# Kernel optimization log

Measured on AMD Instinct MI355X. Metric: run time of the kernel, lower is better.

The kernel has to match this reference:

```python
import jax, jax.numpy as jnp
import numpy as np

B, T, I, H, NSHIFT = 64, 1024, 128, 512, 32


def setup_inputs() -> dict:
    key = jax.random.key(0)
    ks = jax.random.split(key, 8)
    s_in = 1.0 / np.sqrt(I)
    s_h = 1.0 / np.sqrt(H)
    return {
        "x": jax.random.normal(ks[0], (B, T, I), dtype=jnp.float32),
        "W1": jax.random.uniform(ks[1], (I, H), minval=-s_in, maxval=s_in, dtype=jnp.float32),
        "b1": jax.random.uniform(ks[2], (H,), minval=-s_in, maxval=s_in, dtype=jnp.float32),
        "W_ih": jax.random.uniform(ks[3], (H, 4 * H), minval=-s_h, maxval=s_h, dtype=jnp.float32),
        "W_hh": jax.random.uniform(ks[4], (H, 4 * H), minval=-s_h, maxval=s_h, dtype=jnp.float32),
        "b_lstm": jax.random.uniform(ks[5], (4 * H,), minval=-s_h, maxval=s_h, dtype=jnp.float32),
        "Wo": jax.random.uniform(ks[6], (H, NSHIFT), minval=-s_h, maxval=s_h, dtype=jnp.float32),
        "bo": jax.random.uniform(ks[7], (NSHIFT,), minval=-s_h, maxval=s_h, dtype=jnp.float32),
    }


def _lstm_scan(xs, W_ih, W_hh, b, hidden):
    # xs: [T, B, H] (time-major for scan). Sine activation replaces tanh.
    Bsz = xs.shape[1]
    h0 = jnp.zeros((Bsz, hidden), dtype=xs.dtype)
    c0 = jnp.zeros((Bsz, hidden), dtype=xs.dtype)

    def step(carry, xt):
        h, c = carry
        gates = xt @ W_ih + h @ W_hh + b  # [B, 4H]
        i, f, g, o = jnp.split(gates, 4, axis=-1)
        i = jax.nn.sigmoid(i)
        f = jax.nn.sigmoid(f)
        g = jnp.sin(g)  # sine activation in place of tanh
        o = jax.nn.sigmoid(o)
        c_new = f * c + i * g
        h_new = o * jnp.sin(c_new)
        return (h_new, c_new), h_new

    (hT, cT), hs = jax.lax.scan(step, (h0, c0), xs)
    return hs, (hT, cT)


def reference(x, W1, b1, W_ih, W_hh, b_lstm, Wo, bo):
    # fc1: [B, T, I] -> [B, T, H]
    fc1_out = x @ W1 + b1
    xs = jnp.swapaxes(fc1_out, 0, 1)  # [T, B, H]
    hs, _ = _lstm_scan(xs, W_ih, W_hh, b_lstm, W_hh.shape[0])
    lstm_out = jnp.swapaxes(hs, 0, 1)  # [B, T, H]
    return lstm_out @ Wo + bo  # [B, T, n_shift]
```

## Files before the change

### kernel.cpp

```cpp
#include <hip/hip_runtime.h>


constexpr int Bb = 64;
constexpr int Tt = 1024;
constexpr int Ii = 128;
constexpr int Hh = 512;
constexpr int G4 = 2048;
constexpr int NS = 32;
constexpr int NG = 16;
constexpr int GW = 16;
constexpr int BPG = 4;

typedef _Float16 h2 __attribute__((ext_vector_type(2)));
typedef _Float16 h8 __attribute__((ext_vector_type(8)));
typedef float    f4 __attribute__((ext_vector_type(4)));
typedef unsigned int u32;
typedef u32 u32x2 __attribute__((ext_vector_type(2)));
typedef u32 u32x4 __attribute__((ext_vector_type(4)));

__device__ __forceinline__ float dot8(h8 w, h8 x, float acc) {
  h2 w0 = {w[0], w[1]}, w1 = {w[2], w[3]}, w2 = {w[4], w[5]}, w3 = {w[6], w[7]};
  h2 x0 = {x[0], x[1]}, x1 = {x[2], x[3]}, x2 = {x[4], x[5]}, x3 = {x[6], x[7]};
  acc = __builtin_amdgcn_fdot2(x0, w0, acc, false);
  acc = __builtin_amdgcn_fdot2(x1, w1, acc, false);
  acc = __builtin_amdgcn_fdot2(x2, w2, acc, false);
  acc = __builtin_amdgcn_fdot2(x3, w3, acc, false);
  return acc;
}

__device__ __forceinline__ float sigf(float x) { return 1.f / (1.f + __expf(-x)); }


__global__ void k_wc(const float* __restrict__ W1, const float* __restrict__ Wih,
                     const float* __restrict__ b1, const float* __restrict__ bl,
                     _Float16* __restrict__ Wc4, float* __restrict__ bias2) {
  const int j = blockIdx.x;
  const int i = threadIdx.x;
  __shared__ float col[Hh];
  __shared__ float part[128];
  for (int k = i; k < Hh; k += 128) col[k] = Wih[k * G4 + j];
  __syncthreads();
  float s = 0.f;
  for (int k = i; k < Hh; k += 128) s += b1[k] * col[k];
  part[i] = s;
  __syncthreads();
  if (i == 0) {
    float t = bl[j];
    for (int k = 0; k < 128; k++) t += part[k];
    bias2[j] = t;
  }
  float acc = 0.f;
  const float* w1r = W1 + i * Hh;
#pragma unroll 4
  for (int k = 0; k < Hh; k++) acc += w1r[k] * col[k];
  const int gate = j >> 9, r = j & 511, ss = r >> 5, u = r & 31;
  const int c128 = gate * 32 + u, cb = c128 >> 4, c = c128 & 15;
  const int lane = ((i >> 3) & 3) * 16 + c, ks4 = i >> 5, e = i & 7;
  Wc4[((ss * 8 + cb) * 4 + ks4) * 512 + lane * 8 + e] = (_Float16)acc;
}

__global__ void k_whh(const float* __restrict__ W, _Float16* __restrict__ W4) {
  const int id = blockIdx.x * 256 + threadIdx.x;
  const int lane = id & 63, ks = (id >> 6) & 15, cb = (id >> 10) & 7, ss = id >> 13;
  const int c = lane & 15, c128 = cb * 16 + c;
  const int gate = c128 >> 5, u = c128 & 31;
  const int colg = gate * 512 + ss * 32 + u;
  h8 o;
#pragma unroll
  for (int e = 0; e < 8; ++e)
    o[e] = (_Float16)W[(ks * 32 + (lane >> 4) * 8 + e) * G4 + colg];
  *(h8*)(W4 + ((ss * 8 + cb) * 16 + ks) * 512 + lane * 8) = o;
}

__global__ __launch_bounds__(512, 1) void k_scan(
    const float* __restrict__ x, const _Float16* __restrict__ Wc4,
    const float* __restrict__ bias2, const _Float16* __restrict__ Whh4,
    const float* __restrict__ Wo, const float* __restrict__ bo,
    float* __restrict__ out, char* __restrict__ hpub) {
  const int gid = blockIdx.x >> 4, ss = blockIdx.x & 15;
  const int tid = threadIdx.x;
  const int lane = tid & 63, wv = tid >> 6;
  const int l15 = lane & 15, l4 = lane >> 4;

  __shared__ __align__(16) char hls[2][16384];
  __shared__ __align__(16) char xws[4096];
  __shared__ __align__(16) char wots[32768];
  __shared__ float pre_s[2][2][4][4][33];
  __shared__ float gat_s[4][4][33];
  __shared__ float op_s[32][17];

  h8 bW[16], bC[4];
#pragma unroll
  for (int ks = 0; ks < 16; ++ks)
    bW[ks] = *(const h8*)(Whh4 + ((ss * 8 + wv) * 16 + ks) * 512 + lane * 8);
#pragma unroll
  for (int ks = 0; ks < 4; ++ks)
    bC[ks] = *(const h8*)(Wc4 + ((ss * 8 + wv) * 4 + ks) * 512 + lane * 8);

  const int b8 = tid >> 5, ml = tid & 31;
  const float bI = bias2[ss * 32 + ml],        bF = bias2[512 + ss * 32 + ml],
              bG = bias2[1024 + ss * 32 + ml], bO = bias2[1536 + ss * 32 + ml];
  const int nn = tid & 31, pp = tid >> 5;
  const float bor = (tid < NS) ? bo[tid] : 0.f;

#pragma unroll
  for (int q = 0; q < 2; ++q) {
    u32x4 z = {0, 0, 0, 0};
    *(u32x4*)(hls[0] + (q * 512 + tid) * 16) = z;
    *(u32x4*)(hls[1] + (q * 512 + tid) * 16) = z;
  }
  if (tid < 256) { u32x4 z = {0, 0, 0, 0}; *(u32x4*)(xws + tid * 16) = z; }
  for (int it = tid; it < Hh * NS; it += 512) {
    int k = it >> 5, n = it & 31;
    *(_Float16*)(wots + n * 1024 + ((2 * k) ^ ((n & 7) << 4))) = (_Float16)Wo[k * NS + n];
  }
  float c_ = 0.f;

  auto stage_x = [&](int t0) {
    if (tid < 128) {
      const int row = tid >> 4, cc = tid & 15;
      const float* src = x + ((size_t)(gid * BPG + (row & 3)) * Tt + t0 + (row >> 2)) * Ii + cc * 8;
      f4 s0 = *(const f4*)src, s1 = *(const f4*)(src + 4);
      h8 v = {(_Float16)s0[0], (_Float16)s0[1], (_Float16)s0[2], (_Float16)s0[3],
              (_Float16)s1[0], (_Float16)s1[1], (_Float16)s1[2], (_Float16)s1[3]};
      *(h8*)(xws + row * 256 + ((cc * 16) ^ ((row & 7) << 4))) = v;
    }
  };
  auto do_pregate = [&](int buf) {
    f4 pa = {0.f, 0.f, 0.f, 0.f};
#pragma unroll
    for (int ks = 0; ks < 4; ++ks) {
      const int row = l15;
      h8 a = *(const h8*)(xws + row * 256 + ((ks * 64 + l4 * 16) ^ ((row & 7) << 4)));
      pa = __builtin_amdgcn_mfma_f32_16x16x32_f16(a, bC[ks], pa, 0, 0, 0);
    }
    if (l4 < 2) {
      const int c128 = wv * 16 + l15, gam = c128 >> 5, u = c128 & 31;
#pragma unroll
      for (int e = 0; e < 4; ++e) {
        const int row = l4 * 4 + e;
        pre_s[buf][row >> 2][row & 3][gam][u] = pa[e];
      }
    }
  };
  auto op_part = [&](const char* hb) {
    if (ss < BPG) {
      float acc = 0.f;
#pragma unroll
      for (int q = 0; q < 4; ++q) {
        h8 w_ = *(const h8*)(wots + nn * 1024 + ((pp * 64 + q * 16) ^ ((nn & 7) << 4)));
        h8 hv = *(const h8*)(hb + ss * 1024 + ((pp * 64 + q * 16) ^ (ss << 4)));
        acc = dot8(w_, hv, acc);
      }
      op_s[nn][pp] = acc;
    }
  };

  stage_x(0);
  __syncthreads();
  do_pregate(0);

  int cur = 0;
#pragma unroll 1
  for (int t = 0; t < Tt; ++t) {
    char* const hpg = hpub + gid * 16384 + (t & 1) * 8192;
    const char* const hc = hls[cur];
    char* const hn_ = hls[cur ^ 1];
    {
      f4 g0 = {0.f, 0.f, 0.f, 0.f}, g1 = {0.f, 0.f, 0.f, 0.f};
#pragma unroll
      for (int ks = 0; ks < 16; ++ks) {
        const int row = l15;
        h8 a = *(const h8*)(hc + row * 1024 + ((ks * 64 + l4 * 16) ^ (row << 4)));
        if (ks & 1) g1 = __builtin_amdgcn_mfma_f32_16x16x32_f16(a, bW[ks], g1, 0, 0, 0);
        else        g0 = __builtin_amdgcn_mfma_f32_16x16x32_f16(a, bW[ks], g0, 0, 0, 0);
      }
      if (l4 == 0) {
        const int c128 = wv * 16 + l15, gam = c128 >> 5, u = c128 & 31;
#pragma unroll
        for (int e = 0; e < 4; ++e) gat_s[e][gam][u] = g0[e] + g1[e];
      }
    }
    __syncthreads();
    if (tid < 128) {
      const int ph = (t >> 1) & 1, tt = t & 1;
      float aI = gat_s[b8][0][ml] + pre_s[ph][tt][b8][0][ml] + bI;
      float aF = gat_s[b8][1][ml] + pre_s[ph][tt][b8][1][ml] + bF;
      float aG = gat_s[b8][2][ml] + pre_s[ph][tt][b8][2][ml] + bG;
      float aO = gat_s[b8][3][ml] + pre_s[ph][tt][b8][3][ml] + bO;
      float iv = sigf(aI), fv = sigf(aF), gv = __sinf(aG), ov = sigf(aO);
      c_ = fv * c_ + iv * gv;
      float hnv = ov * __sinf(c_);
      _Float16 hf = (_Float16)hnv;
      u32 pkt = (u32)__builtin_bit_cast(unsigned short, hf) | ((u32)(t + 1) << 16);
      u32* dst = (u32*)(hpg + ((size_t)(b8 * 512 + ss * 32 + ml)) * 4);
      asm volatile("global_store_dword %0, %1, off sc0 sc1" :: "v"(dst), "v"(pkt) : "memory");
    }
    if (!(t & 1)) { if (t <= 1020) stage_x(t + 2); }
    else if (t <= 1021) do_pregate(((t + 1) >> 1) & 1);
    if (t > 0) op_part(hc);
    {
      const u32* sp = (const u32*)(hpg + (size_t)tid * 16);
      const u32 want = (u32)(t + 1);
      u32x4 v;
      while (true) {
        asm volatile("global_load_dwordx4 %0, %1, off sc0 sc1\ns_waitcnt vmcnt(0)"
                     : "=v"(v) : "v"(sp) : "memory");
        if ((v[0] >> 16) == want && (v[1] >> 16) == want &&
            (v[2] >> 16) == want && (v[3] >> 16) == want) break;
      }
      __builtin_amdgcn_sched_barrier(0);
      u32x2 d = {(v[0] & 0xFFFFu) | (v[1] << 16), (v[2] & 0xFFFFu) | (v[3] << 16)};
      const int b = tid >> 7, k = tid & 127;
      *(u32x2*)(hn_ + b * 1024 + ((k * 8) ^ (b << 4))) = d;
    }
    __syncthreads();
    if (t > 0 && ss < BPG && tid < NS) {
      float s_ = bor;
#pragma unroll
      for (int p = 0; p < 16; ++p) s_ += op_s[tid][p];
      out[((size_t)(gid * BPG + ss) * Tt + (t - 1)) * NS + tid] = s_;
    }
    cur ^= 1;
  }
  op_part(hls[cur]);
  __syncthreads();
  if (ss < BPG && tid < NS) {
    float s_ = bor;
#pragma unroll
    for (int p = 0; p < 16; ++p) s_ += op_s[tid][p];
    out[((size_t)(gid * BPG + ss) * Tt + 1023) * NS + tid] = s_;
  }
}

extern "C" void kernel_launch(void* const* d_in, const int* in_sizes, int n_in,
                              void* d_out, int out_size, void* d_ws, size_t ws_size,
                              hipStream_t stream) {
  const float* x   = (const float*)d_in[0];
  const float* W1  = (const float*)d_in[1];
  const float* b1  = (const float*)d_in[2];
  const float* Wih = (const float*)d_in[3];
  const float* Whh = (const float*)d_in[4];
  const float* bl  = (const float*)d_in[5];
  const float* Wo  = (const float*)d_in[6];
  const float* bo  = (const float*)d_in[7];
  float* out = (float*)d_out;

  char* ws = (char*)d_ws;
  _Float16* Wc4   = (_Float16*)(ws);
  float*    bias2 = (float*)(ws + 524288);
  _Float16* Whh4  = (_Float16*)(ws + 532480);
  char*     hpub  = ws + 2629632;

  (void)hipMemsetAsync(hpub, 0, 262144, stream);
  k_wc<<<G4, 128, 0, stream>>>(W1, Wih, b1, bl, Wc4, bias2);
  k_whh<<<512, 256, 0, stream>>>(Whh, Whh4);
  k_scan<<<256, 512, 0, stream>>>(x, Wc4, bias2, Whh4, Wo, bo, out, hpub);
}
```

Baseline: 1.906 ms.

## Split recurrent matmul along K across waves, polling h directly into MFMA registers

The recurrent h@W_hh step is repartitioned so that each wave owns a 64-wide K slice across all 128 gate columns. Each wave reads its slice of the previous h directly from the global publish buffer into MFMA A-operands, so the per-step LDS h staging and its full-block poll are gone. Partial gate sums are reduced through LDS before the cell update. The output projection is moved to a separate thread range and lagged by a step, with its own poll into a small LDS buffer, and x staging is moved to other threads so these jobs overlap. This adds a cross-wave reduction, more MFMA accumulators, and polling on only 4 of 16 rows per wave, which wastes MFMA lanes.

```diff
diff --git a/kernel.cpp b/kernel.cpp
--- a/kernel.cpp
+++ b/kernel.cpp
@@ -15,7 +15,6 @@
 typedef _Float16 h8 __attribute__((ext_vector_type(8)));
 typedef float    f4 __attribute__((ext_vector_type(4)));
 typedef unsigned int u32;
-typedef u32 u32x2 __attribute__((ext_vector_type(2)));
 typedef u32 u32x4 __attribute__((ext_vector_type(4)));
 
 __device__ __forceinline__ float dot8(h8 w, h8 x, float acc) {
@@ -29,7 +28,6 @@
 }
 
 __device__ __forceinline__ float sigf(float x) { return 1.f / (1.f + __expf(-x)); }
-
 
 __global__ void k_wc(const float* __restrict__ W1, const float* __restrict__ Wih,
                      const float* __restrict__ b1, const float* __restrict__ bl,
@@ -61,15 +59,16 @@
 
 __global__ void k_whh(const float* __restrict__ W, _Float16* __restrict__ W4) {
   const int id = blockIdx.x * 256 + threadIdx.x;
-  const int lane = id & 63, ks = (id >> 6) & 15, cb = (id >> 10) & 7, ss = id >> 13;
-  const int c = lane & 15, c128 = cb * 16 + c;
+  const int lane = id & 63, ks = (id >> 6) & 1, cb = (id >> 7) & 7;
+  const int wv = (id >> 10) & 7, ss = id >> 13;
+  const int c128 = cb * 16 + (lane & 15);
   const int gate = c128 >> 5, u = c128 & 31;
   const int colg = gate * 512 + ss * 32 + u;
+  const int kbase = wv * 64 + ks * 32 + (lane >> 4) * 8;
   h8 o;
 #pragma unroll
-  for (int e = 0; e < 8; ++e)
-    o[e] = (_Float16)W[(ks * 32 + (lane >> 4) * 8 + e) * G4 + colg];
-  *(h8*)(W4 + ((ss * 8 + cb) * 16 + ks) * 512 + lane * 8) = o;
+  for (int e = 0; e < 8; ++e) o[e] = (_Float16)W[(kbase + e) * G4 + colg];
+  *(h8*)(W4 + ((((ss * 8 + wv) * 8 + cb) * 2 + ks) * 512) + lane * 8) = o;
 }
 
 __global__ __launch_bounds__(512, 1) void k_scan(
@@ -82,34 +81,29 @@
   const int lane = tid & 63, wv = tid >> 6;
   const int l15 = lane & 15, l4 = lane >> 4;
 
-  __shared__ __align__(16) char hls[2][16384];
   __shared__ __align__(16) char xws[4096];
   __shared__ __align__(16) char wots[32768];
   __shared__ float pre_s[2][2][4][4][33];
-  __shared__ float gat_s[4][4][33];
-  __shared__ float op_s[32][17];
-
-  h8 bW[16], bC[4];
-#pragma unroll
-  for (int ks = 0; ks < 16; ++ks)
-    bW[ks] = *(const h8*)(Whh4 + ((ss * 8 + wv) * 16 + ks) * 512 + lane * 8);
+  __shared__ float pgat[8][4][132];
+  __shared__ __align__(16) char hopc[2 * 4 * 1056];
+  __shared__ float op_s[32][9];
+
+  h8 bW[8][2], bC[4];
+#pragma unroll
+  for (int cb = 0; cb < 8; ++cb)
+#pragma unroll
+    for (int ks = 0; ks < 2; ++ks)
+      bW[cb][ks] = *(const h8*)(Whh4 + ((((ss * 8 + wv) * 8 + cb) * 2 + ks) * 512) + lane * 8);
 #pragma unroll
   for (int ks = 0; ks < 4; ++ks)
     bC[ks] = *(const h8*)(Wc4 + ((ss * 8 + wv) * 4 + ks) * 512 + lane * 8);
 
-  const int b8 = tid >> 5, ml = tid & 31;
+  const int cb_ = tid >> 5, ml = tid & 31;
   const float bI = bias2[ss * 32 + ml],        bF = bias2[512 + ss * 32 + ml],
               bG = bias2[1024 + ss * 32 + ml], bO = bias2[1536 + ss * 32 + ml];
-  const int nn = tid & 31, pp = tid >> 5;
   const float bor = (tid < NS) ? bo[tid] : 0.f;
 
-#pragma unroll
-  for (int q = 0; q < 2; ++q) {
-    u32x4 z = {0, 0, 0, 0};
-    *(u32x4*)(hls[0] + (q * 512 + tid) * 16) = z;
-    *(u32x4*)(hls[1] + (q * 512 + tid) * 16) = z;
-  }
-  if (tid < 256) { u32x4 z = {0, 0, 0, 0}; *(u32x4*)(xws + tid * 16) = z; }
+  if (tid < 128) { u32x4 z = {0, 0, 0, 0}; *(u32x4*)(xws + 2048 + tid * 16) = z; }
   for (int it = tid; it < Hh * NS; it += 512) {
     int k = it >> 5, n = it & 31;
     *(_Float16*)(wots + n * 1024 + ((2 * k) ^ ((n & 7) << 4))) = (_Float16)Wo[k * NS + n];
@@ -117,8 +111,8 @@
   float c_ = 0.f;
 
   auto stage_x = [&](int t0) {
-    if (tid < 128) {
-      const int row = tid >> 4, cc = tid & 15;
+    if (tid >= 256 && tid < 384) {
+      const int k = tid - 256, row = k >> 4, cc = k & 15;
       const float* src = x + ((size_t)(gid * BPG + (row & 3)) * Tt + t0 + (row >> 2)) * Ii + cc * 8;
       f4 s0 = *(const f4*)src, s1 = *(const f4*)(src + 4);
       h8 v = {(_Float16)s0[0], (_Float16)s0[1], (_Float16)s0[2], (_Float16)s0[3],
@@ -143,94 +137,160 @@
       }
     }
   };
-  auto op_part = [&](const char* hb) {
-    if (ss < BPG) {
+  auto hop_poll = [&](const char* slot, u32 want, int buf) {
+    if (tid >= 128 && tid < 256) {
+      const int k = tid - 128, row = k >> 5, seg = k & 31;
+      const u32* p = (const u32*)(slot + (row * 512 + seg * 16) * 4);
+      u32x4 v0, v1, v2, v3;
+      while (true) {
+        asm volatile(
+            "global_load_dwordx4 %0, %4, off sc0 sc1\n"
+            "global_load_dwordx4 %1, %5, off sc0 sc1\n"
+            "global_load_dwordx4 %2, %6, off sc0 sc1\n"
+            "global_load_dwordx4 %3, %7, off sc0 sc1\n"
+            "s_waitcnt vmcnt(0)"
+            : "=&v"(v0), "=&v"(v1), "=&v"(v2), "=&v"(v3)
+            : "v"(p), "v"(p + 4), "v"(p + 8), "v"(p + 12)
+            : "memory");
+        if ((v0[0] >> 16) == want && (v0[1] >> 16) == want &&
+            (v0[2] >> 16) == want && (v0[3] >> 16) == want &&
+            (v1[0] >> 16) == want && (v1[1] >> 16) == want &&
+            (v1[2] >> 16) == want && (v1[3] >> 16) == want &&
+            (v2[0] >> 16) == want && (v2[1] >> 16) == want &&
+            (v2[2] >> 16) == want && (v2[3] >> 16) == want &&
+            (v3[0] >> 16) == want && (v3[1] >> 16) == want &&
+            (v3[2] >> 16) == want && (v3[3] >> 16) == want) break;
+      }
+      __builtin_amdgcn_sched_barrier(0);
+      u32x4 w0 = {(v0[0] & 0xffffu) | (v0[1] << 16), (v0[2] & 0xffffu) | (v0[3] << 16),
+                  (v1[0] & 0xffffu) | (v1[1] << 16), (v1[2] & 0xffffu) | (v1[3] << 16)};
+      u32x4 w1 = {(v2[0] & 0xffffu) | (v2[1] << 16), (v2[2] & 0xffffu) | (v2[3] << 16),
+                  (v3[0] & 0xffffu) | (v3[1] << 16), (v3[2] & 0xffffu) | (v3[3] << 16)};
+      const int X = ((seg >> 2) & 7) << 4;
+      char* base = hopc + buf * 4224 + row * 1056;
+      *(u32x4*)(base + ((seg * 32) ^ X)) = w0;
+      *(u32x4*)(base + ((seg * 32 + 16) ^ X)) = w1;
+    }
+  };
+  auto opf = [&](int buf) {
+    if (ss < BPG && tid >= 256) {
+      const int k = tid - 256, nn = k & 31, pp = k >> 5;
       float acc = 0.f;
 #pragma unroll
-      for (int q = 0; q < 4; ++q) {
-        h8 w_ = *(const h8*)(wots + nn * 1024 + ((pp * 64 + q * 16) ^ ((nn & 7) << 4)));
-        h8 hv = *(const h8*)(hb + ss * 1024 + ((pp * 64 + q * 16) ^ (ss << 4)));
+      for (int q = 0; q < 8; ++q) {
+        const int off = pp * 128 + q * 16;
+        h8 w_ = *(const h8*)(wots + nn * 1024 + (off ^ ((nn & 7) << 4)));
+        h8 hv = *(const h8*)(hopc + buf * 4224 + ss * 1056 + (off ^ ((pp & 7) << 4)));
         acc = dot8(w_, hv, acc);
       }
       op_s[nn][pp] = acc;
     }
   };
+  auto out_store = [&](int tindex) {
+    if (ss < BPG && tid < NS) {
+      float s_ = bor;
+#pragma unroll
+      for (int p = 0; p < 8; ++p) s_ += op_s[tid][p];
+      out[((size_t)(gid * BPG + ss) * Tt + tindex) * NS + tid] = s_;
+    }
+  };
 
   stage_x(0);
   __syncthreads();
   do_pregate(0);
 
-  int cur = 0;
 #pragma unroll 1
   for (int t = 0; t < Tt; ++t) {
-    char* const hpg = hpub + gid * 16384 + (t & 1) * 8192;
-    const char* const hc = hls[cur];
-    char* const hn_ = hls[cur ^ 1];
+    const char* slotP = hpub + gid * 16384 + ((t - 1) & 1) * 8192;
+    char* slotC = hpub + gid * 16384 + (t & 1) * 8192;
+    if (t >= 3) out_store(t - 3);
+    if (t & 1) { if (t <= 1021) do_pregate(((t + 1) >> 1) & 1); }
+    else if (t <= 1020) stage_x(t + 2);
     {
-      f4 g0 = {0.f, 0.f, 0.f, 0.f}, g1 = {0.f, 0.f, 0.f, 0.f};
-#pragma unroll
-      for (int ks = 0; ks < 16; ++ks) {
-        const int row = l15;
-        h8 a = *(const h8*)(hc + row * 1024 + ((ks * 64 + l4 * 16) ^ (row << 4)));
-        if (ks & 1) g1 = __builtin_amdgcn_mfma_f32_16x16x32_f16(a, bW[ks], g1, 0, 0, 0);
-        else        g0 = __builtin_amdgcn_mfma_f32_16x16x32_f16(a, bW[ks], g0, 0, 0, 0);
+      f4 acc[8] = {{0.f,0.f,0.f,0.f},{0.f,0.f,0.f,0.f},{0.f,0.f,0.f,0.f},{0.f,0.f,0.f,0.f},
+                   {0.f,0.f,0.f,0.f},{0.f,0.f,0.f,0.f},{0.f,0.f,0.f,0.f},{0.f,0.f,0.f,0.f}};
+      if (t > 0) {
+        h8 a0 = {}, a1 = {};
+        if (l15 < 4) {
+          const u32* p = (const u32*)(slotP + (l15 * 512 + wv * 64 + l4 * 8) * 4);
+          const u32 want = (u32)t;
+          u32x4 v0, v1, v2, v3;
+          while (true) {
+            asm volatile(
+                "global_load_dwordx4 %0, %4, off sc0 sc1\n"
+                "global_load_dwordx4 %1, %5, off sc0 sc1\n"
+                "global_load_dwordx4 %2, %6, off sc0 sc1\n"
+                "global_load_dwordx4 %3, %7, off sc0 sc1\n"
+                "s_waitcnt vmcnt(0)"
+                : "=&v"(v0), "=&v"(v1), "=&v"(v2), "=&v"(v3)
+                : "v"(p), "v"(p + 4), "v"(p + 32), "v"(p + 36)
+                : "memory");
+            if ((v0[0] >> 16) == want && (v0[1] >> 16) == want &&
+                (v0[2] >> 16) == want && (v0[3] >> 16) == want &&
+                (v1[0] >> 16) == want && (v1[1] >> 16) == want &&
+                (v1[2] >> 16) == want && (v1[3] >> 16) == want &&
+                (v2[0] >> 16) == want && (v2[1] >> 16) == want &&
+                (v2[2] >> 16) == want && (v2[3] >> 16) == want &&
+                (v3[0] >> 16) == want && (v3[1] >> 16) == want &&
+                (v3[2] >> 16) == want && (v3[3] >> 16) == want) break;
+          }
+          __builtin_amdgcn_sched_barrier(0);
+          u32x4 w0 = {(v0[0] & 0xffffu) | (v0[1] << 16), (v0[2] & 0xffffu) | (v0[3] << 16),
+                      (v1[0] & 0xffffu) | (v1[1] << 16), (v1[2] & 0xffffu) | (v1[3] << 16)};
+          u32x4 w1 = {(v2[0] & 0xffffu) | (v2[1] << 16), (v2[2] & 0xffffu) | (v2[3] << 16),
+                      (v3[0] & 0xffffu) | (v3[1] << 16), (v3[2] & 0xffffu) | (v3[3] << 16)};
+          a0 = __builtin_bit_cast(h8, w0);
+          a1 = __builtin_bit_cast(h8, w1);
+        }
+#pragma unroll
+        for (int cb = 0; cb < 8; ++cb) {
+          acc[cb] = __builtin_amdgcn_mfma_f32_16x16x32_f16(a0, bW[cb][0], acc[cb], 0, 0, 0);
+          acc[cb] = __builtin_amdgcn_mfma_f32_16x16x32_f16(a1, bW[cb][1], acc[cb], 0, 0, 0);
+        }
       }
       if (l4 == 0) {
-        const int c128 = wv * 16 + l15, gam = c128 >> 5, u = c128 & 31;
-#pragma unroll
-        for (int e = 0; e < 4; ++e) gat_s[e][gam][u] = g0[e] + g1[e];
-      }
-    }
+#pragma unroll
+        for (int cb = 0; cb < 8; ++cb)
+#pragma unroll
+          for (int e = 0; e < 4; ++e)
+            pgat[wv][e][cb * 16 + l15] = acc[cb][e];
+      }
+    }
+    if (t >= 1) hop_poll(slotP, (u32)t, t & 1);
     __syncthreads();
     if (tid < 128) {
-      const int ph = (t >> 1) & 1, tt = t & 1;
-      float aI = gat_s[b8][0][ml] + pre_s[ph][tt][b8][0][ml] + bI;
-      float aF = gat_s[b8][1][ml] + pre_s[ph][tt][b8][1][ml] + bF;
-      float aG = gat_s[b8][2][ml] + pre_s[ph][tt][b8][2][ml] + bG;
-      float aO = gat_s[b8][3][ml] + pre_s[ph][tt][b8][3][ml] + bO;
+      const int b = cb_, u = ml, ph = (t >> 1) & 1, tt = t & 1;
+      float s0 = 0.f, s1 = 0.f, s2 = 0.f, s3 = 0.f;
+#pragma unroll
+      for (int w = 0; w < 8; ++w) {
+        s0 += pgat[w][b][u];       s1 += pgat[w][b][32 + u];
+        s2 += pgat[w][b][64 + u];  s3 += pgat[w][b][96 + u];
+      }
+      float aI = s0 + pre_s[ph][tt][b][0][u] + bI;
+      float aF = s1 + pre_s[ph][tt][b][1][u] + bF;
+      float aG = s2 + pre_s[ph][tt][b][2][u] + bG;
+      float aO = s3 + pre_s[ph][tt][b][3][u] + bO;
       float iv = sigf(aI), fv = sigf(aF), gv = __sinf(aG), ov = sigf(aO);
       c_ = fv * c_ + iv * gv;
       float hnv = ov * __sinf(c_);
       _Float16 hf = (_Float16)hnv;
       u32 pkt = (u32)__builtin_bit_cast(unsigned short, hf) | ((u32)(t + 1) << 16);
-      u32* dst = (u32*)(hpg + ((size_t)(b8 * 512 + ss * 32 + ml)) * 4);
+      u32* dst = (u32*)(slotC + ((size_t)(b * 512 + ss * 32 + u)) * 4);
       asm volatile("global_store_dword %0, %1, off sc0 sc1" :: "v"(dst), "v"(pkt) : "memory");
     }
-    if (!(t & 1)) { if (t <= 1020) stage_x(t + 2); }
-    else if (t <= 1021) do_pregate(((t + 1) >> 1) & 1);
-    if (t > 0) op_part(hc);
-    {
-      const u32* sp = (const u32*)(hpg + (size_t)tid * 16);
-      const u32 want = (u32)(t + 1);
-      u32x4 v;
-      while (true) {
-        asm volatile("global_load_dwordx4 %0, %1, off sc0 sc1\ns_waitcnt vmcnt(0)"
-                     : "=v"(v) : "v"(sp) : "memory");
-        if ((v[0] >> 16) == want && (v[1] >> 16) == want &&
-            (v[2] >> 16) == want && (v[3] >> 16) == want) break;
-      }
-      __builtin_amdgcn_sched_barrier(0);
-      u32x2 d = {(v[0] & 0xFFFFu) | (v[1] << 16), (v[2] & 0xFFFFu) | (v[3] << 16)};
-      const int b = tid >> 7, k = tid & 127;
-      *(u32x2*)(hn_ + b * 1024 + ((k * 8) ^ (b << 4))) = d;
-    }
+    if (t >= 2) opf((t - 1) & 1);
     __syncthreads();
-    if (t > 0 && ss < BPG && tid < NS) {
-      float s_ = bor;
-#pragma unroll
-      for (int p = 0; p < 16; ++p) s_ += op_s[tid][p];
-      out[((size_t)(gid * BPG + ss) * Tt + (t - 1)) * NS + tid] = s_;
-    }
-    cur ^= 1;
   }
-  op_part(hls[cur]);
-  __syncthreads();
-  if (ss < BPG && tid < NS) {
-    float s_ = bor;
-#pragma unroll
-    for (int p = 0; p < 16; ++p) s_ += op_s[tid][p];
-    out[((size_t)(gid * BPG + ss) * Tt + 1023) * NS + tid] = s_;
-  }
+  out_store(1021);
+  __syncthreads();
+  opf(1);
+  __syncthreads();
+  out_store(1022);
+  hop_poll(hpub + gid * 16384 + 8192, (u32)1024, 0);
+  __syncthreads();
+  opf(0);
+  __syncthreads();
+  out_store(1023);
 }
 
 extern "C" void kernel_launch(void* const* d_in, const int* in_sizes, int n_in,
```

Result: slower. 2.700 ms (+41.6%).

## Interleave gate columns per unit and compute cell update in-register via shuffles

Applied to the files above, without the earlier changes.

The Whh and fused input weight column layouts now interleave the four gates of each hidden unit across adjacent lanes, so the MFMA output for one unit lands in four neighbouring lanes. Lane shuffles gather the i/f/g/o values into one lane, which then does the cell update directly. This removes the gate LDS staging array and one __syncthreads per timestep from the serial recurrence. The output-projection partials are double-buffered to stay safe with the remaining barrier. The cost is more shuffle instructions, and each cell lane now handles four batch rows serially with four global stores.

```diff
diff --git a/kernel.cpp b/kernel.cpp
--- a/kernel.cpp
+++ b/kernel.cpp
@@ -54,22 +54,22 @@
 #pragma unroll 4
   for (int k = 0; k < Hh; k++) acc += w1r[k] * col[k];
   const int gate = j >> 9, r = j & 511, ss = r >> 5, u = r & 31;
-  const int c128 = gate * 32 + u, cb = c128 >> 4, c = c128 & 15;
-  const int lane = ((i >> 3) & 3) * 16 + c, ks4 = i >> 5, e = i & 7;
-  Wc4[((ss * 8 + cb) * 4 + ks4) * 512 + lane * 8 + e] = (_Float16)acc;
+  const int wv = u >> 2, ul = u & 3;
+  const int l15 = ul * 4 + gate;
+  const int ks4 = i >> 5, l4 = (i >> 3) & 3, e = i & 7;
+  Wc4[((ss * 8 + wv) * 4 + ks4) * 512 + (l4 * 16 + l15) * 8 + e] = (_Float16)acc;
 }
 
 __global__ void k_whh(const float* __restrict__ W, _Float16* __restrict__ W4) {
   const int id = blockIdx.x * 256 + threadIdx.x;
-  const int lane = id & 63, ks = (id >> 6) & 15, cb = (id >> 10) & 7, ss = id >> 13;
-  const int c = lane & 15, c128 = cb * 16 + c;
-  const int gate = c128 >> 5, u = c128 & 31;
-  const int colg = gate * 512 + ss * 32 + u;
+  const int lane = id & 63, ks = (id >> 6) & 15, wv = (id >> 10) & 7, ss = id >> 13;
+  const int l15 = lane & 15, gate = l15 & 3, ul = l15 >> 2;
+  const int colg = gate * 512 + ss * 32 + wv * 4 + ul;
   h8 o;
 #pragma unroll
   for (int e = 0; e < 8; ++e)
     o[e] = (_Float16)W[(ks * 32 + (lane >> 4) * 8 + e) * G4 + colg];
-  *(h8*)(W4 + ((ss * 8 + cb) * 16 + ks) * 512 + lane * 8) = o;
+  *(h8*)(W4 + ((ss * 8 + wv) * 16 + ks) * 512 + lane * 8) = o;
 }
 
 __global__ __launch_bounds__(512, 1) void k_scan(
@@ -81,13 +81,16 @@
   const int tid = threadIdx.x;
   const int lane = tid & 63, wv = tid >> 6;
   const int l15 = lane & 15, l4 = lane >> 4;
+  const int ul = l15 >> 2;
+  const bool cellLane = (l4 == 0) && ((l15 & 3) == 0);
+  const int unitW = wv * 4 + ul;
+  const int gunit = ss * 32 + unitW;
 
   __shared__ __align__(16) char hls[2][16384];
   __shared__ __align__(16) char xws[4096];
   __shared__ __align__(16) char wots[32768];
-  __shared__ float pre_s[2][2][4][4][33];
-  __shared__ float gat_s[4][4][33];
-  __shared__ float op_s[32][17];
+  __shared__ __align__(16) float pre_s[2][32][36];
+  __shared__ float op_s[2][32][17];
 
   h8 bW[16], bC[4];
 #pragma unroll
@@ -97,10 +100,12 @@
   for (int ks = 0; ks < 4; ++ks)
     bC[ks] = *(const h8*)(Wc4 + ((ss * 8 + wv) * 4 + ks) * 512 + lane * 8);
 
-  const int b8 = tid >> 5, ml = tid & 31;
-  const float bI = bias2[ss * 32 + ml],        bF = bias2[512 + ss * 32 + ml],
-              bG = bias2[1024 + ss * 32 + ml], bO = bias2[1536 + ss * 32 + ml];
-  const int nn = tid & 31, pp = tid >> 5;
+  float bIr = 0.f, bFr = 0.f, bGr = 0.f, bOr = 0.f;
+  if (cellLane) {
+    bIr = bias2[gunit];        bFr = bias2[512 + gunit];
+    bGr = bias2[1024 + gunit]; bOr = bias2[1536 + gunit];
+  }
+  f4 c4 = {0.f, 0.f, 0.f, 0.f};
   const float bor = (tid < NS) ? bo[tid] : 0.f;
 
 #pragma unroll
@@ -114,7 +119,6 @@
     int k = it >> 5, n = it & 31;
     *(_Float16*)(wots + n * 1024 + ((2 * k) ^ ((n & 7) << 4))) = (_Float16)Wo[k * NS + n];
   }
-  float c_ = 0.f;
 
   auto stage_x = [&](int t0) {
     if (tid < 128) {
@@ -134,17 +138,24 @@
       h8 a = *(const h8*)(xws + row * 256 + ((ks * 64 + l4 * 16) ^ ((row & 7) << 4)));
       pa = __builtin_amdgcn_mfma_f32_16x16x32_f16(a, bC[ks], pa, 0, 0, 0);
     }
-    if (l4 < 2) {
-      const int c128 = wv * 16 + l15, gam = c128 >> 5, u = c128 & 31;
-#pragma unroll
-      for (int e = 0; e < 4; ++e) {
-        const int row = l4 * 4 + e;
-        pre_s[buf][row >> 2][row & 3][gam][u] = pa[e];
-      }
-    }
-  };
-  auto op_part = [&](const char* hb) {
+    f4 q1, q2, q3;
+#pragma unroll
+    for (int e = 0; e < 4; ++e) q1[e] = __shfl_xor(pa[e], 1);
+#pragma unroll
+    for (int e = 0; e < 4; ++e) q2[e] = __shfl_xor(pa[e], 2);
+#pragma unroll
+    for (int e = 0; e < 4; ++e) q3[e] = __shfl_xor(q1[e], 2);
+    if (((l15 & 3) == 0) && l4 < 2) {
+      float* pw = &pre_s[buf][unitW][l4 * 16];
+      *(f4*)(pw)      = pa;
+      *(f4*)(pw + 4)  = q1;
+      *(f4*)(pw + 8)  = q2;
+      *(f4*)(pw + 12) = q3;
+    }
+  };
+  auto op_part = [&](const char* hb, int buf) {
     if (ss < BPG) {
+      const int nn = tid & 31, pp = tid >> 5;
       float acc = 0.f;
 #pragma unroll
       for (int q = 0; q < 4; ++q) {
@@ -152,7 +163,15 @@
         h8 hv = *(const h8*)(hb + ss * 1024 + ((pp * 64 + q * 16) ^ (ss << 4)));
         acc = dot8(w_, hv, acc);
       }
-      op_s[nn][pp] = acc;
+      op_s[buf][nn][pp] = acc;
+    }
+  };
+  auto out_store = [&](int tindex, int buf) {
+    if (ss < BPG && tid < NS) {
+      float s_ = bor;
+#pragma unroll
+      for (int p = 0; p < 16; ++p) s_ += op_s[buf][tid][p];
+      out[((size_t)(gid * BPG + ss) * Tt + tindex) * NS + tid] = s_;
     }
   };
 
@@ -166,39 +185,53 @@
     char* const hpg = hpub + gid * 16384 + (t & 1) * 8192;
     const char* const hc = hls[cur];
     char* const hn_ = hls[cur ^ 1];
-    {
-      f4 g0 = {0.f, 0.f, 0.f, 0.f}, g1 = {0.f, 0.f, 0.f, 0.f};
-#pragma unroll
-      for (int ks = 0; ks < 16; ++ks) {
-        const int row = l15;
-        h8 a = *(const h8*)(hc + row * 1024 + ((ks * 64 + l4 * 16) ^ (row << 4)));
-        if (ks & 1) g1 = __builtin_amdgcn_mfma_f32_16x16x32_f16(a, bW[ks], g1, 0, 0, 0);
-        else        g0 = __builtin_amdgcn_mfma_f32_16x16x32_f16(a, bW[ks], g0, 0, 0, 0);
-      }
-      if (l4 == 0) {
-        const int c128 = wv * 16 + l15, gam = c128 >> 5, u = c128 & 31;
-#pragma unroll
-        for (int e = 0; e < 4; ++e) gat_s[e][gam][u] = g0[e] + g1[e];
-      }
-    }
-    __syncthreads();
-    if (tid < 128) {
-      const int ph = (t >> 1) & 1, tt = t & 1;
-      float aI = gat_s[b8][0][ml] + pre_s[ph][tt][b8][0][ml] + bI;
-      float aF = gat_s[b8][1][ml] + pre_s[ph][tt][b8][1][ml] + bF;
-      float aG = gat_s[b8][2][ml] + pre_s[ph][tt][b8][2][ml] + bG;
-      float aO = gat_s[b8][3][ml] + pre_s[ph][tt][b8][3][ml] + bO;
-      float iv = sigf(aI), fv = sigf(aF), gv = __sinf(aG), ov = sigf(aO);
-      c_ = fv * c_ + iv * gv;
-      float hnv = ov * __sinf(c_);
-      _Float16 hf = (_Float16)hnv;
-      u32 pkt = (u32)__builtin_bit_cast(unsigned short, hf) | ((u32)(t + 1) << 16);
-      u32* dst = (u32*)(hpg + ((size_t)(b8 * 512 + ss * 32 + ml)) * 4);
-      asm volatile("global_store_dword %0, %1, off sc0 sc1" :: "v"(dst), "v"(pkt) : "memory");
+    f4 g0 = {0.f, 0.f, 0.f, 0.f}, g1 = {0.f, 0.f, 0.f, 0.f};
+#pragma unroll
+    for (int ks = 0; ks < 16; ++ks) {
+      const int row = l15;
+      h8 a = *(const h8*)(hc + row * 1024 + ((ks * 64 + l4 * 16) ^ (row << 4)));
+      if (ks & 1) g1 = __builtin_amdgcn_mfma_f32_16x16x32_f16(a, bW[ks], g1, 0, 0, 0);
+      else        g0 = __builtin_amdgcn_mfma_f32_16x16x32_f16(a, bW[ks], g0, 0, 0, 0);
+    }
+    f4 gs;
+#pragma unroll
+    for (int e = 0; e < 4; ++e) gs[e] = g0[e] + g1[e];
+    f4 v1, v2, v3;
+#pragma unroll
+    for (int e = 0; e < 4; ++e) v1[e] = __shfl_xor(gs[e], 1);
+#pragma unroll
+    for (int e = 0; e < 4; ++e) v2[e] = __shfl_xor(gs[e], 2);
+#pragma unroll
+    for (int e = 0; e < 4; ++e) v3[e] = __shfl_xor(v1[e], 2);
+    if (cellLane) {
+      const int tt = t & 1, ph = (t >> 1) & 1;
+      const float* pr = &pre_s[ph][unitW][tt * 16];
+      f4 pI = *(const f4*)(pr);
+      f4 pF = *(const f4*)(pr + 4);
+      f4 pG = *(const f4*)(pr + 8);
+      f4 pO = *(const f4*)(pr + 12);
+      u32 pkts[4];
+#pragma unroll
+      for (int e = 0; e < 4; ++e) {
+        float aI = gs[e] + pI[e] + bIr;
+        float aF = v1[e] + pF[e] + bFr;
+        float aG = v2[e] + pG[e] + bGr;
+        float aO = v3[e] + pO[e] + bOr;
+        float iv = sigf(aI), fv = sigf(aF), gv = __sinf(aG), ov = sigf(aO);
+        c4[e] = fv * c4[e] + iv * gv;
+        float hnv = ov * __sinf(c4[e]);
+        _Float16 hf = (_Float16)hnv;
+        pkts[e] = (u32)__builtin_bit_cast(unsigned short, hf) | ((u32)(t + 1) << 16);
+      }
+#pragma unroll
+      for (int e = 0; e < 4; ++e) {
+        u32* dst = (u32*)(hpg + ((size_t)(e * 512 + gunit)) * 4);
+        asm volatile("global_store_dword %0, %1, off sc0 sc1" :: "v"(dst), "v"(pkts[e]) : "memory");
+      }
     }
     if (!(t & 1)) { if (t <= 1020) stage_x(t + 2); }
     else if (t <= 1021) do_pregate(((t + 1) >> 1) & 1);
-    if (t > 0) op_part(hc);
+    if (t > 0) op_part(hc, t & 1);
     {
       const u32* sp = (const u32*)(hpg + (size_t)tid * 16);
       const u32 want = (u32)(t + 1);
@@ -215,22 +248,12 @@
       *(u32x2*)(hn_ + b * 1024 + ((k * 8) ^ (b << 4))) = d;
     }
     __syncthreads();
-    if (t > 0 && ss < BPG && tid < NS) {
-      float s_ = bor;
-#pragma unroll
-      for (int p = 0; p < 16; ++p) s_ += op_s[tid][p];
-      out[((size_t)(gid * BPG + ss) * Tt + (t - 1)) * NS + tid] = s_;
-    }
+    if (t > 0) out_store(t - 1, t & 1);
     cur ^= 1;
   }
-  op_part(hls[cur]);
-  __syncthreads();
-  if (ss < BPG && tid < NS) {
-    float s_ = bor;
-#pragma unroll
-    for (int p = 0; p < 16; ++p) s_ += op_s[tid][p];
-    out[((size_t)(gid * BPG + ss) * Tt + 1023) * NS + tid] = s_;
-  }
+  op_part(hls[cur], 0);
+  __syncthreads();
+  out_store(1023, 0);
 }
 
 extern "C" void kernel_launch(void* const* d_in, const int* in_sizes, int n_in,
```

New measurement: 3.206 ms. 68.2% more time.

## Process two batch sub-groups per block to halve grid and interleave recurrences

Applied to the files above, without the earlier changes.

Each block now handles 8 batch rows as two independent 4-row sub-groups (A and B), and the grid shrinks from 256 to 128 blocks. The two recurrent GEMMs and cell updates are interleaved so one sub-group's publish and poll latency can overlap with the other's compute. Because the same Whh register tiles serve both sub-groups, each block does more work per cross-block synchronization round. The cost is double the LDS for h buffers, an extra barrier per step, and more serial MFMA work per block, so per-step latency may rise.

```diff
diff --git a/kernel.cpp b/kernel.cpp
--- a/kernel.cpp
+++ b/kernel.cpp
@@ -7,9 +7,9 @@
 constexpr int Hh = 512;
 constexpr int G4 = 2048;
 constexpr int NS = 32;
-constexpr int NG = 16;
+constexpr int NG = 8;
 constexpr int GW = 16;
-constexpr int BPG = 4;
+constexpr int BPG = 8;
 
 typedef _Float16 h2 __attribute__((ext_vector_type(2)));
 typedef _Float16 h8 __attribute__((ext_vector_type(8)));
@@ -82,12 +82,14 @@
   const int lane = tid & 63, wv = tid >> 6;
   const int l15 = lane & 15, l4 = lane >> 4;
 
-  __shared__ __align__(16) char hls[2][16384];
+  __shared__ __align__(16) char hlsA[2][16384];
+  __shared__ __align__(16) char hlsB[2][16384];
   __shared__ __align__(16) char xws[4096];
   __shared__ __align__(16) char wots[32768];
-  __shared__ float pre_s[2][2][4][4][33];
-  __shared__ float gat_s[4][4][33];
-  __shared__ float op_s[32][17];
+  __shared__ __align__(16) float pre_s[2][2][8][4][33];
+  __shared__ float gatA[4][4][33];
+  __shared__ float gatB[4][4][33];
+  __shared__ float op_s[2][32][17];
 
   h8 bW[16], bC[4];
 #pragma unroll
@@ -97,29 +99,32 @@
   for (int ks = 0; ks < 4; ++ks)
     bC[ks] = *(const h8*)(Wc4 + ((ss * 8 + wv) * 4 + ks) * 512 + lane * 8);
 
-  const int b8 = tid >> 5, ml = tid & 31;
-  const float bI = bias2[ss * 32 + ml],        bF = bias2[512 + ss * 32 + ml],
-              bG = bias2[1024 + ss * 32 + ml], bO = bias2[1536 + ss * 32 + ml];
-  const int nn = tid & 31, pp = tid >> 5;
+  const int cu = tid & 31;
+  float bI = 0.f, bF = 0.f, bG = 0.f, bO = 0.f;
+  if (tid < 256) {
+    bI = bias2[ss * 32 + cu];        bF = bias2[512 + ss * 32 + cu];
+    bG = bias2[1024 + ss * 32 + cu]; bO = bias2[1536 + ss * 32 + cu];
+  }
+  float c_ = 0.f;
   const float bor = (tid < NS) ? bo[tid] : 0.f;
 
 #pragma unroll
   for (int q = 0; q < 2; ++q) {
     u32x4 z = {0, 0, 0, 0};
-    *(u32x4*)(hls[0] + (q * 512 + tid) * 16) = z;
-    *(u32x4*)(hls[1] + (q * 512 + tid) * 16) = z;
-  }
-  if (tid < 256) { u32x4 z = {0, 0, 0, 0}; *(u32x4*)(xws + tid * 16) = z; }
+    *(u32x4*)(hlsA[0] + (q * 512 + tid) * 16) = z;
+    *(u32x4*)(hlsA[1] + (q * 512 + tid) * 16) = z;
+    *(u32x4*)(hlsB[0] + (q * 512 + tid) * 16) = z;
+    *(u32x4*)(hlsB[1] + (q * 512 + tid) * 16) = z;
+  }
   for (int it = tid; it < Hh * NS; it += 512) {
     int k = it >> 5, n = it & 31;
     *(_Float16*)(wots + n * 1024 + ((2 * k) ^ ((n & 7) << 4))) = (_Float16)Wo[k * NS + n];
   }
-  float c_ = 0.f;
 
   auto stage_x = [&](int t0) {
-    if (tid < 128) {
+    if (tid < 256) {
       const int row = tid >> 4, cc = tid & 15;
-      const float* src = x + ((size_t)(gid * BPG + (row & 3)) * Tt + t0 + (row >> 2)) * Ii + cc * 8;
+      const float* src = x + ((size_t)(gid * BPG + (row & 7)) * Tt + t0 + (row >> 3)) * Ii + cc * 8;
       f4 s0 = *(const f4*)src, s1 = *(const f4*)(src + 4);
       h8 v = {(_Float16)s0[0], (_Float16)s0[1], (_Float16)s0[2], (_Float16)s0[3],
               (_Float16)s1[0], (_Float16)s1[1], (_Float16)s1[2], (_Float16)s1[3]};
@@ -134,26 +139,79 @@
       h8 a = *(const h8*)(xws + row * 256 + ((ks * 64 + l4 * 16) ^ ((row & 7) << 4)));
       pa = __builtin_amdgcn_mfma_f32_16x16x32_f16(a, bC[ks], pa, 0, 0, 0);
     }
-    if (l4 < 2) {
-      const int c128 = wv * 16 + l15, gam = c128 >> 5, u = c128 & 31;
-#pragma unroll
-      for (int e = 0; e < 4; ++e) {
-        const int row = l4 * 4 + e;
-        pre_s[buf][row >> 2][row & 3][gam][u] = pa[e];
-      }
-    }
-  };
-  auto op_part = [&](const char* hb) {
+    const int c128 = wv * 16 + l15, gam = c128 >> 5, u = c128 & 31;
+#pragma unroll
+    for (int e = 0; e < 4; ++e) {
+      const int row = l4 * 4 + e;
+      pre_s[buf][row >> 3][row & 7][gam][u] = pa[e];
+    }
+  };
+  auto op_part = [&](const char* hAc, const char* hBc, int buf) {
     if (ss < BPG) {
+      const char* hb = (ss < 4 ? hAc : hBc) + (ss & 3) * 1024;
+      const int r = ss & 3;
+      const int nn = tid & 31, pp = tid >> 5;
       float acc = 0.f;
 #pragma unroll
       for (int q = 0; q < 4; ++q) {
         h8 w_ = *(const h8*)(wots + nn * 1024 + ((pp * 64 + q * 16) ^ ((nn & 7) << 4)));
-        h8 hv = *(const h8*)(hb + ss * 1024 + ((pp * 64 + q * 16) ^ (ss << 4)));
+        h8 hv = *(const h8*)(hb + ((pp * 64 + q * 16) ^ (r << 4)));
         acc = dot8(w_, hv, acc);
       }
-      op_s[nn][pp] = acc;
-    }
+      op_s[buf][nn][pp] = acc;
+    }
+  };
+  auto out_store = [&](int tindex, int buf) {
+    if (ss < BPG && tid < NS) {
+      float s_ = bor;
+#pragma unroll
+      for (int p = 0; p < 16; ++p) s_ += op_s[buf][tid][p];
+      out[((size_t)(gid * BPG + ss) * Tt + tindex) * NS + tid] = s_;
+    }
+  };
+  auto gemm = [&](const char* hc, float (*gat)[4][33]) {
+    f4 g0 = {0.f, 0.f, 0.f, 0.f}, g1 = {0.f, 0.f, 0.f, 0.f};
+#pragma unroll
+    for (int ks = 0; ks < 16; ++ks) {
+      const int row = l15;
+      h8 a = *(const h8*)(hc + row * 1024 + ((ks * 64 + l4 * 16) ^ (row << 4)));
+      if (ks & 1) g1 = __builtin_amdgcn_mfma_f32_16x16x32_f16(a, bW[ks], g1, 0, 0, 0);
+      else        g0 = __builtin_amdgcn_mfma_f32_16x16x32_f16(a, bW[ks], g0, 0, 0, 0);
+    }
+    if (l4 == 0) {
+      const int c128 = wv * 16 + l15, gam = c128 >> 5, u = c128 & 31;
+#pragma unroll
+      for (int e = 0; e < 4; ++e) gat[e][gam][u] = g0[e] + g1[e];
+    }
+  };
+  auto cell_pub = [&](float (*gat)[4][33], int bloc, int t, char* slot) {
+    const int tt = t & 1, ph = (t >> 1) & 1;
+    const int bp = (tid < 128 ? 0 : 4) + bloc;
+    float aI = gat[bloc][0][cu] + pre_s[ph][tt][bp][0][cu] + bI;
+    float aF = gat[bloc][1][cu] + pre_s[ph][tt][bp][1][cu] + bF;
+    float aG = gat[bloc][2][cu] + pre_s[ph][tt][bp][2][cu] + bG;
+    float aO = gat[bloc][3][cu] + pre_s[ph][tt][bp][3][cu] + bO;
+    float iv = sigf(aI), fv = sigf(aF), gv = __sinf(aG), ov = sigf(aO);
+    c_ = fv * c_ + iv * gv;
+    float hnv = ov * __sinf(c_);
+    _Float16 hf = (_Float16)hnv;
+    u32 pkt = (u32)__builtin_bit_cast(unsigned short, hf) | ((u32)(t + 1) << 16);
+    u32* dst = (u32*)(slot + ((size_t)(bloc * 512 + ss * 32 + cu)) * 4);
+    asm volatile("global_store_dword %0, %1, off sc0 sc1" :: "v"(dst), "v"(pkt) : "memory");
+  };
+  auto poll_restage = [&](const char* slot, char* hn_, u32 want) {
+    const u32* sp = (const u32*)(slot + (size_t)tid * 16);
+    u32x4 v;
+    while (true) {
+      asm volatile("global_load_dwordx4 %0, %1, off sc0 sc1\ns_waitcnt vmcnt(0)"
+                   : "=v"(v) : "v"(sp) : "memory");
+      if ((v[0] >> 16) == want && (v[1] >> 16) == want &&
+          (v[2] >> 16) == want && (v[3] >> 16) == want) break;
+    }
+    __builtin_amdgcn_sched_barrier(0);
+    u32x2 d = {(v[0] & 0xFFFFu) | (v[1] << 16), (v[2] & 0xFFFFu) | (v[3] << 16)};
+    const int b = tid >> 7, k = tid & 127;
+    *(u32x2*)(hn_ + b * 1024 + ((k * 8) ^ (b << 4))) = d;
   };
 
   stage_x(0);
@@ -163,74 +221,26 @@
   int cur = 0;
 #pragma unroll 1
   for (int t = 0; t < Tt; ++t) {
-    char* const hpg = hpub + gid * 16384 + (t & 1) * 8192;
-    const char* const hc = hls[cur];
-    char* const hn_ = hls[cur ^ 1];
-    {
-      f4 g0 = {0.f, 0.f, 0.f, 0.f}, g1 = {0.f, 0.f, 0.f, 0.f};
-#pragma unroll
-      for (int ks = 0; ks < 16; ++ks) {
-        const int row = l15;
-        h8 a = *(const h8*)(hc + row * 1024 + ((ks * 64 + l4 * 16) ^ (row << 4)));
-        if (ks & 1) g1 = __builtin_amdgcn_mfma_f32_16x16x32_f16(a, bW[ks], g1, 0, 0, 0);
-        else        g0 = __builtin_amdgcn_mfma_f32_16x16x32_f16(a, bW[ks], g0, 0, 0, 0);
-      }
-      if (l4 == 0) {
-        const int c128 = wv * 16 + l15, gam = c128 >> 5, u = c128 & 31;
-#pragma unroll
-        for (int e = 0; e < 4; ++e) gat_s[e][gam][u] = g0[e] + g1[e];
-      }
-    }
+    char* const slotA = hpub + ((gid * 2 + 0) * 2 + (t & 1)) * 8192;
+    char* const slotB = hpub + ((gid * 2 + 1) * 2 + (t & 1)) * 8192;
+    gemm(hlsA[cur], gatA);
     __syncthreads();
-    if (tid < 128) {
-      const int ph = (t >> 1) & 1, tt = t & 1;
-      float aI = gat_s[b8][0][ml] + pre_s[ph][tt][b8][0][ml] + bI;
-      float aF = gat_s[b8][1][ml] + pre_s[ph][tt][b8][1][ml] + bF;
-      float aG = gat_s[b8][2][ml] + pre_s[ph][tt][b8][2][ml] + bG;
-      float aO = gat_s[b8][3][ml] + pre_s[ph][tt][b8][3][ml] + bO;
-      float iv = sigf(aI), fv = sigf(aF), gv = __sinf(aG), ov = sigf(aO);
-      c_ = fv * c_ + iv * gv;
-      float hnv = ov * __sinf(c_);
-      _Float16 hf = (_Float16)hnv;
-      u32 pkt = (u32)__builtin_bit_cast(unsigned short, hf) | ((u32)(t + 1) << 16);
-      u32* dst = (u32*)(hpg + ((size_t)(b8 * 512 + ss * 32 + ml)) * 4);
-      asm volatile("global_store_dword %0, %1, off sc0 sc1" :: "v"(dst), "v"(pkt) : "memory");
-    }
+    if (tid < 128) cell_pub(gatA, tid >> 5, t, slotA);
+    gemm(hlsB[cur], gatB);
+    __syncthreads();
+    if (tid >= 128 && tid < 256) cell_pub(gatB, (tid - 128) >> 5, t, slotB);
     if (!(t & 1)) { if (t <= 1020) stage_x(t + 2); }
     else if (t <= 1021) do_pregate(((t + 1) >> 1) & 1);
-    if (t > 0) op_part(hc);
-    {
-      const u32* sp = (const u32*)(hpg + (size_t)tid * 16);
-      const u32 want = (u32)(t + 1);
-      u32x4 v;
-      while (true) {
-        asm volatile("global_load_dwordx4 %0, %1, off sc0 sc1\ns_waitcnt vmcnt(0)"
-                     : "=v"(v) : "v"(sp) : "memory");
-        if ((v[0] >> 16) == want && (v[1] >> 16) == want &&
-            (v[2] >> 16) == want && (v[3] >> 16) == want) break;
-      }
-      __builtin_amdgcn_sched_barrier(0);
-      u32x2 d = {(v[0] & 0xFFFFu) | (v[1] << 16), (v[2] & 0xFFFFu) | (v[3] << 16)};
-      const int b = tid >> 7, k = tid & 127;
-      *(u32x2*)(hn_ + b * 1024 + ((k * 8) ^ (b << 4))) = d;
-    }
+    if (t > 0) op_part(hlsA[cur], hlsB[cur], t & 1);
+    poll_restage(slotA, hlsA[cur ^ 1], (u32)(t + 1));
+    poll_restage(slotB, hlsB[cur ^ 1], (u32)(t + 1));
     __syncthreads();
-    if (t > 0 && ss < BPG && tid < NS) {
-      float s_ = bor;
-#pragma unroll
-      for (int p = 0; p < 16; ++p) s_ += op_s[tid][p];
-      out[((size_t)(gid * BPG + ss) * Tt + (t - 1)) * NS + tid] = s_;
-    }
+    if (t > 0) out_store(t - 1, t & 1);
     cur ^= 1;
   }
-  op_part(hls[cur]);
-  __syncthreads();
-  if (ss < BPG && tid < NS) {
-    float s_ = bor;
-#pragma unroll
-    for (int p = 0; p < 16; ++p) s_ += op_s[tid][p];
-    out[((size_t)(gid * BPG + ss) * Tt + 1023) * NS + tid] = s_;
-  }
+  op_part(hlsA[cur], hlsB[cur], 0);
+  __syncthreads();
+  out_store(1023, 0);
 }
 
 extern "C" void kernel_launch(void* const* d_in, const int* in_sizes, int n_in,
@@ -255,5 +265,5 @@
   (void)hipMemsetAsync(hpub, 0, 262144, stream);
   k_wc<<<G4, 128, 0, stream>>>(W1, Wih, b1, bl, Wc4, bias2);
   k_whh<<<512, 256, 0, stream>>>(Whh, Whh4);
-  k_scan<<<256, 512, 0, stream>>>(x, Wc4, bias2, Whh4, Wo, bo, out, hpub);
-}
+  k_scan<<<NG * GW, 512, 0, stream>>>(x, Wc4, bias2, Whh4, Wo, bo, out, hpub);
+}
```

New measurement: 2.334 ms. +22.5%, slower.
